# Performance work log

Measured on AMD Instinct MI355X. Metric: run time of the kernel, lower is better.

Reference implementation:

```python
import jax, jax.numpy as jnp
import numpy as np

B, N = 256, 65536          # batch, num_tokens (world.num_tokens == N)
VOCAB = 50257
ALPHA = 0.5                # dirichlet concentration
EPS = 1e-7                 # gumbel eps


def setup_inputs() -> dict:
    key = jax.random.key(0)
    kb, kt, ku, kd = jax.random.split(key, 4)
    batch = jax.random.randint(kb, (B, N), 0, VOCAB, dtype=jnp.int32)
    t = jax.random.uniform(kt, (B,), dtype=jnp.float32)
    U = jax.random.uniform(ku, (B, N), dtype=jnp.float32)
    # dirichlet(alpha=0.5) sample over the token axis, one simplex per row
    D = jax.random.dirichlet(kd, ALPHA * jnp.ones((N,), jnp.float32), shape=(B,)).astype(jnp.float32)
    return {"batch": batch, "t": t, "U": U, "D": D}


def cosine_schedule(t):
    return 1.0 - jnp.cos(jnp.pi * t / 2)


def cosine_weight(t, eps=1e-3):
    t_adj = t * (1 - 2 * eps) + eps
    return 0.5 * jnp.pi * jnp.sin(jnp.pi * t_adj / 2)


def binary_topk(weights, ks):
    # weights: [B, N] float; ks: [B, 1] int -> bool mask marking the top-k per row
    Bn, Nn = weights.shape
    idx = jnp.argsort(-weights, axis=-1)                     # descending order indices
    rank = jnp.broadcast_to(jnp.arange(Nn), (Bn, Nn))        # rank of each sorted slot
    mask = jnp.zeros((Bn, Nn), dtype=bool)
    mask = mask.at[jnp.arange(Bn)[:, None], idx].set(ks > rank)
    return mask


def reference(batch, t, U, D):
    r = cosine_schedule(t)                                   # mask rate per sample [B]
    w = cosine_weight(t)                                     # loss weight per sample [B]
    G = -jnp.log(-jnp.log(U + EPS) + EPS)                    # gumbel noise [B, N]
    weights = G + jnp.log(D)                                 # gumbel + log-dirichlet
    ks = (N * r).astype(jnp.int32)[:, None]                  # [B, 1] tokens to mask
    mask = binary_topk(weights, ks)                          # [B, N] bool
    return mask, w
```

## Files before the change

kernel.cpp:

```cpp
#include <hip/hip_runtime.h>
#include <math.h>

#define BB 256
#define NN 65536
#define NT 1024
#define CAP 2016
#define MARGIN 2e-3f

typedef float f32x4 __attribute__((ext_vector_type(4)));
typedef unsigned int u32x4 __attribute__((ext_vector_type(4)));

#define ONE_BITS 0x3F800000u

__device__ __forceinline__ unsigned int f2sort(float f) {
    unsigned int b = __float_as_uint(f);
    return (b & 0x80000000u) ? ~b : (b | 0x80000000u);
}
__device__ __forceinline__ float sort2f(unsigned int u) {
    unsigned int b = (u & 0x80000000u) ? (u & 0x7fffffffu) : ~u;
    return __uint_as_float(b);
}

__device__ __forceinline__ unsigned int wexact(float u, float d) {
    float t1 = u + 1e-7f;
    float t2 = (float)log((double)t1);
    float t3 = (-t2) + 1e-7f;
    float G  = -(float)log((double)t3);
    float lgD = (float)log((double)d);
    return f2sort(G + lgD);
}

__device__ __forceinline__ unsigned int wfast(float u, float d) {
    float t1 = u + 1e-7f;
    float t3 = -__logf(t1) + 1e-7f;
    float G  = -__logf(t3);
    return f2sort(G + __logf(d));
}

__device__ __forceinline__ bool finite_f(float f) {
    return (__float_as_uint(f) & 0x7f800000u) != 0x7f800000u;
}

#define PASS1SEL(KKV) \
    { const int b0 = tid * 8; unsigned int cs = 0; \
      _Pragma("unroll") for (int i = 0; i < 8; i++) cs += hist[b0 + i]; \
      chunkSum[tid] = cs; } \
    __syncthreads(); \
    if (tid < 64) { \
        const int c0i = lane * 16; unsigned int s = 0; \
        _Pragma("unroll") for (int i = 0; i < 16; i++) s += chunkSum[c0i + i]; \
        unsigned int suf = s; \
        _Pragma("unroll") for (int off = 1; off < 64; off <<= 1) { \
            unsigned int tv = __shfl_down(suf, off); if (lane + off < 64) suf += tv; } \
        unsigned int above = suf - s; \
        if (suf >= (KKV) && above < (KKV)) { \
            unsigned int cum = above; \
            for (int ci = c0i + 15; ci >= c0i; ci--) { \
                unsigned int cch = chunkSum[ci]; \
                if (cum + cch >= (KKV)) { \
                    for (int b = ci * 8 + 7; ; b--) { \
                        unsigned int c2 = hist[b]; \
                        if (cum + c2 >= (KKV)) { s_sel = (unsigned int)b; s_kneed = (KKV) - cum; s_eq = c2; break; } \
                        cum += c2; } \
                    break; } \
                cum += cch; } } } \
    __syncthreads();

#define PASS2SEL(P, KN) \
    if (tid < 64) { \
        const int c0i = lane * 16; unsigned int s = 0; \
        _Pragma("unroll") for (int i = 0; i < 16; i++) s += hist[c0i + i]; \
        unsigned int suf = s; \
        _Pragma("unroll") for (int off = 1; off < 64; off <<= 1) { \
            unsigned int tv = __shfl_down(suf, off); if (lane + off < 64) suf += tv; } \
        unsigned int above = suf - s; \
        if (suf >= (KN) && above < (KN)) { \
            unsigned int cum = above; \
            for (int b = c0i + 15; ; b--) { \
                unsigned int c2 = hist[b]; \
                if (cum + c2 >= (KN)) { s_sel = ((P) << 10) | (unsigned int)b; s_kneed = (KN) - cum; s_eq = c2; break; } \
                cum += c2; } } } \
    __syncthreads();

#define PASS3SEL(P, KN) \
    if (tid < 64) { \
        const int c0i = lane * 8; unsigned int s = 0; \
        _Pragma("unroll") for (int i = 0; i < 8; i++) s += hist[c0i + i]; \
        unsigned int suf = s; \
        _Pragma("unroll") for (int off = 1; off < 64; off <<= 1) { \
            unsigned int tv = __shfl_down(suf, off); if (lane + off < 64) suf += tv; } \
        unsigned int above = suf - s; \
        if (suf >= (KN) && above < (KN)) { \
            unsigned int cum = above; \
            for (int b = c0i + 7; ; b--) { \
                unsigned int c2 = hist[b]; \
                if (cum + c2 >= (KN)) { s_sel = ((P) << 9) | (unsigned int)b; s_kneed = (KN) - cum; s_eq = c2; break; } \
                cum += c2; } } } \
    __syncthreads();

__global__ __launch_bounds__(NT, 4)
void md_fused_kernel(const float* __restrict__ Tt,
                     const float* __restrict__ U,
                     const float* __restrict__ D,
                     float* __restrict__ out,
                     float* __restrict__ wout) {
    const int row = blockIdx.x;
    const int tid = threadIdx.x;
    const int lane = tid & 63;

    const float* Ur = U + (size_t)row * NN;
    const float* Dr = D + (size_t)row * NN;
    unsigned int* OrU = (unsigned int*)out + (size_t)row * NN;

    __shared__ unsigned int hist[8192];
    __shared__ unsigned int chunkSum[NT];
    __shared__ unsigned int bandU[CAP];
    __shared__ int bandIdx[CAP];
    __shared__ unsigned int s_sel, s_kneed, s_eq;
    __shared__ int s_A, s_bandCnt, s_tiecnt, s_tieidx;

    int* tielist = bandIdx;

    const float t = Tt[row];
    const float pf = (float)M_PI;
    float aa = pf * t;
    float bbv = aa * 0.5f;
    float c0 = (float)cos((double)bbv);
    float r  = 1.0f - c0;
    const int k = (int)(65536.0f * r);
    if (tid == 0) {
        float tadj = t * 0.998f + 0.001f;
        float arg  = (pf * tadj) * 0.5f;
        wout[row] = (float)(0.5 * M_PI) * (float)sin((double)arg);
    }

    if (k <= 0 || k >= NN) {
        const unsigned int fb = (k >= NN) ? ONE_BITS : 0u;
        u32x4 f4 = {fb, fb, fb, fb};
        for (int j = 0; j < 16; j++)
            __builtin_nontemporal_store(f4, (u32x4*)(OrU + j * 4096 + tid * 4));
        return;
    }
    const unsigned int kk = (unsigned int)k;

    for (int i = tid; i < 8192; i += NT) hist[i] = 0;
    if (tid == 0) { s_A = 0; s_bandCnt = 0; }
    __syncthreads();

#pragma unroll 2
    for (int J = 0; J < 16; ++J) {
        const int e = (J << 12) + (tid << 2);
        float4 u4 = *(const float4*)(Ur + e);
        float4 d4 = *(const float4*)(Dr + e);
        u32x4 kv;
        kv.x = wfast(u4.x, d4.x);
        kv.y = wfast(u4.y, d4.y);
        kv.z = wfast(u4.z, d4.z);
        kv.w = wfast(u4.w, d4.w);
        *(u32x4*)(OrU + e) = kv;
        atomicAdd(&hist[kv.x >> 19], 1u);
        atomicAdd(&hist[kv.y >> 19], 1u);
        atomicAdd(&hist[kv.z >> 19], 1u);
        atomicAdd(&hist[kv.w >> 19], 1u);
    }
    __syncthreads();

    PASS1SEL(kk)
    const unsigned int p13 = s_sel;
    const unsigned int kn1 = s_kneed;
    hist[tid] = 0;
    __syncthreads();

#pragma unroll 2
    for (int J = 0; J < 16; ++J) {
        const int e = (J << 12) + (tid << 2);
        u32x4 kv = *(const u32x4*)(OrU + e);
        if ((kv.x >> 19) == p13) atomicAdd(&hist[(kv.x >> 9) & 1023u], 1u);
        if ((kv.y >> 19) == p13) atomicAdd(&hist[(kv.y >> 9) & 1023u], 1u);
        if ((kv.z >> 19) == p13) atomicAdd(&hist[(kv.z >> 9) & 1023u], 1u);
        if ((kv.w >> 19) == p13) atomicAdd(&hist[(kv.w >> 9) & 1023u], 1u);
    }
    __syncthreads();
    PASS2SEL(p13, kn1)

    const unsigned int p23 = s_sel;
    const float loF = sort2f(p23 << 9) - MARGIN;
    const float hiF = sort2f((p23 << 9) | 511u) + MARGIN;
    const bool badBand = !(finite_f(loF) && finite_f(hiF));
    const unsigned int lo_u = f2sort(loF);
    const unsigned int hi_u = f2sort(hiF);

    {
        int cnt = 0;
#pragma unroll 2
        for (int J = 0; J < 16; ++J) {
            const int e = (J << 12) + (tid << 2);
            u32x4 kv = __builtin_nontemporal_load((const u32x4*)(OrU + e));
            u32x4 m;
#define MRGV(UU, EIDX, MF) { const unsigned int uu = (UU); \
            const bool din = uu > hi_u; cnt += (int)din; MF = din ? ONE_BITS : 0u; \
            if (!din && uu >= lo_u) { \
                int slot = atomicAdd(&s_bandCnt, 1); \
                if (slot < CAP) bandIdx[slot] = (EIDX); } }
            MRGV(kv.x, e + 0, m.x)
            MRGV(kv.y, e + 1, m.y)
            MRGV(kv.z, e + 2, m.z)
            MRGV(kv.w, e + 3, m.w)
#undef MRGV
            __builtin_nontemporal_store(m, (u32x4*)(OrU + e));
        }
#pragma unroll
        for (int off = 32; off >= 1; off >>= 1) cnt += __shfl_down(cnt, off);
        if (lane == 0) atomicAdd(&s_A, cnt);
    }
    __syncthreads();

    const int bandCnt = s_bandCnt;
    const int kb = k - s_A;
    const bool fallback = badBand || (bandCnt > CAP) || (kb < 0) || (kb > bandCnt);

    if (!fallback) {
        for (int j = tid; j < bandCnt; j += NT) {
            int idx = bandIdx[j];
            bandU[j] = wexact(Ur[idx], Dr[idx]);
        }
        __syncthreads();
        for (int j = tid; j < bandCnt; j += NT) {
            unsigned int me = bandU[j];
            int mi = bandIdx[j];
            int rk = 0;
            for (int i = 0; i < bandCnt; i++) {
                unsigned int o = bandU[i];
                rk += (int)((o > me) || (o == me && bandIdx[i] < mi));
            }
            if (rk < kb) OrU[mi] = ONE_BITS;
        }
        return;
    }

    __syncthreads();
    for (int i = tid; i < 8192; i += NT) hist[i] = 0;
    __syncthreads();
#pragma unroll 1
    for (int J = 0; J < 16; ++J) {
        const int e = (J << 12) + (tid << 2);
        float4 u4 = *(const float4*)(Ur + e);
        float4 d4 = *(const float4*)(Dr + e);
        u32x4 kv;
        kv.x = wexact(u4.x, d4.x);
        kv.y = wexact(u4.y, d4.y);
        kv.z = wexact(u4.z, d4.z);
        kv.w = wexact(u4.w, d4.w);
        *(u32x4*)(OrU + e) = kv;
        atomicAdd(&hist[kv.x >> 19], 1u);
        atomicAdd(&hist[kv.y >> 19], 1u);
        atomicAdd(&hist[kv.z >> 19], 1u);
        atomicAdd(&hist[kv.w >> 19], 1u);
    }
    __syncthreads();

    PASS1SEL(kk)
    const unsigned int q13 = s_sel;
    const unsigned int en1 = s_kneed;
    hist[tid] = 0;
    __syncthreads();
#pragma unroll 1
    for (int J = 0; J < 16; ++J) {
        const int e = (J << 12) + (tid << 2);
        u32x4 kv = *(const u32x4*)(OrU + e);
        if ((kv.x >> 19) == q13) atomicAdd(&hist[(kv.x >> 9) & 1023u], 1u);
        if ((kv.y >> 19) == q13) atomicAdd(&hist[(kv.y >> 9) & 1023u], 1u);
        if ((kv.z >> 19) == q13) atomicAdd(&hist[(kv.z >> 9) & 1023u], 1u);
        if ((kv.w >> 19) == q13) atomicAdd(&hist[(kv.w >> 9) & 1023u], 1u);
    }
    __syncthreads();
    PASS2SEL(q13, en1)

    const unsigned int q23 = s_sel;
    const unsigned int en2 = s_kneed;
    if (tid < 512) hist[tid] = 0;
    __syncthreads();
#pragma unroll 1
    for (int J = 0; J < 16; ++J) {
        const int e = (J << 12) + (tid << 2);
        u32x4 kv = *(const u32x4*)(OrU + e);
        if ((kv.x >> 9) == q23) atomicAdd(&hist[kv.x & 511u], 1u);
        if ((kv.y >> 9) == q23) atomicAdd(&hist[kv.y & 511u], 1u);
        if ((kv.z >> 9) == q23) atomicAdd(&hist[kv.z & 511u], 1u);
        if ((kv.w >> 9) == q23) atomicAdd(&hist[kv.w & 511u], 1u);
    }
    __syncthreads();
    PASS3SEL(q23, en2)

    const unsigned int theta = s_sel;
    const unsigned int kneedF = s_kneed, eqF = s_eq;
    const bool needOrder = (kneedF < eqF);
    int istar = NN;
    if (needOrder) {
        if (tid == 0) s_tiecnt = 0;
        __syncthreads();
#pragma unroll 1
        for (int J = 0; J < 16; ++J) {
            const int e = (J << 12) + (tid << 2);
            u32x4 kv = *(const u32x4*)(OrU + e);
#define TIEV(UU, EIDX) if ((UU) == theta) { \
                int pos = atomicAdd(&s_tiecnt, 1); \
                if (pos < 1024) tielist[pos] = (EIDX); }
            TIEV(kv.x, e + 0)
            TIEV(kv.y, e + 1)
            TIEV(kv.z, e + 2)
            TIEV(kv.w, e + 3)
#undef TIEV
        }
        __syncthreads();
        if (tid == 0) {
            int E = s_tiecnt; if (E > 1024) E = 1024;
            for (int aI = 1; aI < E; aI++) {
                int val = tielist[aI]; int bI = aI - 1;
                while (bI >= 0 && tielist[bI] > val) { tielist[bI + 1] = tielist[bI]; bI--; }
                tielist[bI + 1] = val;
            }
            int kk2 = (int)kneedF; if (kk2 > E) kk2 = E; if (kk2 < 1) kk2 = 1;
            s_tieidx = tielist[kk2 - 1];
        }
        __syncthreads();
        istar = s_tieidx;
    }

#pragma unroll 1
    for (int J = 0; J < 16; ++J) {
        const int e = (J << 12) + (tid << 2);
        u32x4 kv = __builtin_nontemporal_load((const u32x4*)(OrU + e));
        u32x4 m;
#define MVE(u, idx) ((((u) > theta) || ((u) == theta && (!needOrder || (idx) <= istar))) ? ONE_BITS : 0u)
        m.x = MVE(kv.x, e + 0);
        m.y = MVE(kv.y, e + 1);
        m.z = MVE(kv.z, e + 2);
        m.w = MVE(kv.w, e + 3);
#undef MVE
        __builtin_nontemporal_store(m, (u32x4*)(OrU + e));
    }
}

extern "C" void kernel_launch(void* const* d_in, const int* in_sizes, int n_in,
                              void* d_out, int out_size, void* d_ws, size_t ws_size,
                              hipStream_t stream) {
    const float* T = (const float*)d_in[1];
    const float* U = (const float*)d_in[2];
    const float* D = (const float*)d_in[3];
    float* out = (float*)d_out;
    float* wout = out + (size_t)BB * NN;

    md_fused_kernel<<<BB, NT, 0, stream>>>(T, U, D, out, wout);
}
```

Baseline: 233.5 us.

## Select top-k via sampled pivots and monotone ratio key with candidate compaction

Replaces the gumbel+log-dirichlet key with a monotone-equivalent ratio key d/(-log(u)) that needs only one fast log and a reciprocal. Instead of two full passes writing and rereading keys in global memory, it samples the first 4096 elements to estimate high and low rank pivots, then makes one streaming pass that writes the mask for definitely-selected elements and wave-compacts candidates into shared memory. Exact selection within the candidates uses a radix select followed by an exact-key brute-force rank on a narrow band. This removes global key writes and rereads but adds sampling overhead and more fallback conditions. It also relies on the sample being representative.

```diff
diff --git a/kernel.cpp b/kernel.cpp
--- a/kernel.cpp
+++ b/kernel.cpp
@@ -4,8 +4,11 @@
 #define BB 256
 #define NN 65536
 #define NT 1024
-#define CAP 2016
-#define MARGIN 2e-3f
+#define SM 4096
+#define RANKPAD 160
+#define CAPC 8192
+#define CAPB 2048
+#define QMARG 2e-3f
 
 typedef float f32x4 __attribute__((ext_vector_type(4)));
 typedef unsigned int u32x4 __attribute__((ext_vector_type(4)));
@@ -30,11 +33,10 @@
     return f2sort(G + lgD);
 }
 
-__device__ __forceinline__ unsigned int wfast(float u, float d) {
-    float t1 = u + 1e-7f;
-    float t3 = -__logf(t1) + 1e-7f;
-    float G  = -__logf(t3);
-    return f2sort(G + __logf(d));
+__device__ __forceinline__ unsigned int qkey(float u, float d) {
+    float t3 = 1e-7f - __logf(u + 1e-7f);
+    float q  = d * __builtin_amdgcn_rcpf(t3);
+    return f2sort(q);
 }
 
 __device__ __forceinline__ bool finite_f(float f) {
@@ -114,12 +116,15 @@
 
     __shared__ unsigned int hist[8192];
     __shared__ unsigned int chunkSum[NT];
-    __shared__ unsigned int bandU[CAP];
-    __shared__ int bandIdx[CAP];
+    __shared__ unsigned int skey[SM];
+    __shared__ unsigned int candKey[CAPC];
+    __shared__ int candIdx[CAPC];
     __shared__ unsigned int s_sel, s_kneed, s_eq;
-    __shared__ int s_A, s_bandCnt, s_tiecnt, s_tieidx;
-
-    int* tielist = bandIdx;
+    __shared__ int s_A, s_candCnt, s_bandCnt, s_above, s_tiecnt, s_tieidx;
+
+    unsigned int* bandU = skey;
+    int* bandIdxA = (int*)(skey + CAPB);
+    int* tielist = candIdx;
 
     const float t = Tt[row];
     const float pf = (float)M_PI;
@@ -135,8 +140,8 @@
     }
 
     if (k <= 0 || k >= NN) {
-        const unsigned int fb = (k >= NN) ? ONE_BITS : 0u;
-        u32x4 f4 = {fb, fb, fb, fb};
+        const unsigned int fbv = (k >= NN) ? ONE_BITS : 0u;
+        u32x4 f4 = {fbv, fbv, fbv, fbv};
         for (int j = 0; j < 16; j++)
             __builtin_nontemporal_store(f4, (u32x4*)(OrU + j * 4096 + tid * 4));
         return;
@@ -144,98 +149,168 @@
     const unsigned int kk = (unsigned int)k;
 
     for (int i = tid; i < 8192; i += NT) hist[i] = 0;
-    if (tid == 0) { s_A = 0; s_bandCnt = 0; }
-    __syncthreads();
-
-#pragma unroll 2
-    for (int J = 0; J < 16; ++J) {
-        const int e = (J << 12) + (tid << 2);
-        float4 u4 = *(const float4*)(Ur + e);
-        float4 d4 = *(const float4*)(Dr + e);
-        u32x4 kv;
-        kv.x = wfast(u4.x, d4.x);
-        kv.y = wfast(u4.y, d4.y);
-        kv.z = wfast(u4.z, d4.z);
-        kv.w = wfast(u4.w, d4.w);
-        *(u32x4*)(OrU + e) = kv;
-        atomicAdd(&hist[kv.x >> 19], 1u);
-        atomicAdd(&hist[kv.y >> 19], 1u);
-        atomicAdd(&hist[kv.z >> 19], 1u);
-        atomicAdd(&hist[kv.w >> 19], 1u);
-    }
-    __syncthreads();
-
-    PASS1SEL(kk)
-    const unsigned int p13 = s_sel;
-    const unsigned int kn1 = s_kneed;
-    hist[tid] = 0;
-    __syncthreads();
-
-#pragma unroll 2
-    for (int J = 0; J < 16; ++J) {
-        const int e = (J << 12) + (tid << 2);
-        u32x4 kv = *(const u32x4*)(OrU + e);
-        if ((kv.x >> 19) == p13) atomicAdd(&hist[(kv.x >> 9) & 1023u], 1u);
-        if ((kv.y >> 19) == p13) atomicAdd(&hist[(kv.y >> 9) & 1023u], 1u);
-        if ((kv.z >> 19) == p13) atomicAdd(&hist[(kv.z >> 9) & 1023u], 1u);
-        if ((kv.w >> 19) == p13) atomicAdd(&hist[(kv.w >> 9) & 1023u], 1u);
-    }
-    __syncthreads();
-    PASS2SEL(p13, kn1)
-
-    const unsigned int p23 = s_sel;
-    const float loF = sort2f(p23 << 9) - MARGIN;
-    const float hiF = sort2f((p23 << 9) | 511u) + MARGIN;
-    const bool badBand = !(finite_f(loF) && finite_f(hiF));
-    const unsigned int lo_u = f2sort(loF);
-    const unsigned int hi_u = f2sort(hiF);
-
+    if (tid == 0) { s_A = 0; s_candCnt = 0; s_bandCnt = 0; s_above = 0; }
+    __syncthreads();
     {
-        int cnt = 0;
+        float4 u4 = *(const float4*)(Ur + (tid << 2));
+        float4 d4 = *(const float4*)(Dr + (tid << 2));
+        unsigned int s0 = qkey(u4.x, d4.x), s1 = qkey(u4.y, d4.y);
+        unsigned int s2 = qkey(u4.z, d4.z), s3 = qkey(u4.w, d4.w);
+        skey[(tid << 2) + 0] = s0; skey[(tid << 2) + 1] = s1;
+        skey[(tid << 2) + 2] = s2; skey[(tid << 2) + 3] = s3;
+        atomicAdd(&hist[s0 >> 19], 1u); atomicAdd(&hist[s1 >> 19], 1u);
+        atomicAdd(&hist[s2 >> 19], 1u); atomicAdd(&hist[s3 >> 19], 1u);
+    }
+    __syncthreads();
+
+    const int rh = (k >> 4) - RANKPAD;
+    unsigned int hi_pivot_u = 0xFFFFFFFFu;
+    if (rh >= 1) {
+        PASS1SEL((unsigned int)rh)
+        const unsigned int bh = s_sel; const unsigned int knh = s_kneed;
+        hist[tid] = 0;
+        __syncthreads();
+        for (int j = tid; j < SM; j += NT) { unsigned int sk = skey[j];
+            if ((sk >> 19) == bh) atomicAdd(&hist[(sk >> 9) & 1023u], 1u); }
+        __syncthreads();
+        PASS2SEL(bh, knh)
+        hi_pivot_u = (s_sel << 9) | 0x1FFu;
+        for (int i = tid; i < 8192; i += NT) hist[i] = 0;
+        __syncthreads();
+        for (int j = tid; j < SM; j += NT) atomicAdd(&hist[skey[j] >> 19], 1u);
+        __syncthreads();
+    }
+
+    const int rl = ((k + 15) >> 4) + RANKPAD;
+    unsigned int lo_pivot_u = 0u;
+    if (rl <= SM) {
+        PASS1SEL((unsigned int)rl)
+        const unsigned int bl = s_sel; const unsigned int knl = s_kneed;
+        hist[tid] = 0;
+        __syncthreads();
+        for (int j = tid; j < SM; j += NT) { unsigned int sk = skey[j];
+            if ((sk >> 19) == bl) atomicAdd(&hist[(sk >> 9) & 1023u], 1u); }
+        __syncthreads();
+        PASS2SEL(bl, knl)
+        lo_pivot_u = (s_sel << 9);
+    }
+    __syncthreads();
+
+    {
+        int cntA = 0;
 #pragma unroll 2
         for (int J = 0; J < 16; ++J) {
             const int e = (J << 12) + (tid << 2);
-            u32x4 kv = __builtin_nontemporal_load((const u32x4*)(OrU + e));
+            float4 u4 = *(const float4*)(Ur + e);
+            float4 d4 = *(const float4*)(Dr + e);
+            u32x4 kv;
+            kv.x = qkey(u4.x, d4.x); kv.y = qkey(u4.y, d4.y);
+            kv.z = qkey(u4.z, d4.z); kv.w = qkey(u4.w, d4.w);
             u32x4 m;
-#define MRGV(UU, EIDX, MF) { const unsigned int uu = (UU); \
-            const bool din = uu > hi_u; cnt += (int)din; MF = din ? ONE_BITS : 0u; \
-            if (!din && uu >= lo_u) { \
-                int slot = atomicAdd(&s_bandCnt, 1); \
-                if (slot < CAP) bandIdx[slot] = (EIDX); } }
-            MRGV(kv.x, e + 0, m.x)
-            MRGV(kv.y, e + 1, m.y)
-            MRGV(kv.z, e + 2, m.z)
-            MRGV(kv.w, e + 3, m.w)
-#undef MRGV
-            __builtin_nontemporal_store(m, (u32x4*)(OrU + e));
+#define MPROC(KC, CI, MF) { \
+            const unsigned int qv = (KC); \
+            const bool din = qv > hi_pivot_u; \
+            cntA += (int)din; MF = din ? ONE_BITS : 0u; \
+            const bool isc = (!din) && (qv > lo_pivot_u); \
+            const unsigned long long mb = __ballot(isc); \
+            if (mb) { \
+                const int ldr = __ffsll((unsigned long long)mb) - 1; \
+                int wbase = 0; \
+                if (lane == ldr) wbase = atomicAdd(&s_candCnt, __popcll(mb)); \
+                wbase = __shfl(wbase, ldr); \
+                if (isc) { \
+                    const int slot = wbase + __popcll(mb & ((1ull << lane) - 1ull)); \
+                    if (slot < CAPC) { candKey[slot] = qv; candIdx[slot] = e + (CI); } \
+                } } }
+            MPROC(kv.x, 0, m.x)
+            MPROC(kv.y, 1, m.y)
+            MPROC(kv.z, 2, m.z)
+            MPROC(kv.w, 3, m.w)
+#undef MPROC
+            *(u32x4*)(OrU + e) = m;
         }
 #pragma unroll
-        for (int off = 32; off >= 1; off >>= 1) cnt += __shfl_down(cnt, off);
-        if (lane == 0) atomicAdd(&s_A, cnt);
-    }
-    __syncthreads();
-
-    const int bandCnt = s_bandCnt;
+        for (int off = 32; off >= 1; off >>= 1) cntA += __shfl_down(cntA, off);
+        if (lane == 0) atomicAdd(&s_A, cntA);
+    }
+    __syncthreads();
+
+    const int candCnt0 = s_candCnt;
+    const int candCnt = candCnt0 > CAPC ? CAPC : candCnt0;
     const int kb = k - s_A;
-    const bool fallback = badBand || (bandCnt > CAP) || (kb < 0) || (kb > bandCnt);
-
-    if (!fallback) {
-        for (int j = tid; j < bandCnt; j += NT) {
-            int idx = bandIdx[j];
-            bandU[j] = wexact(Ur[idx], Dr[idx]);
+    bool fb = (candCnt0 > CAPC) || (kb < 1) || (kb > candCnt0);
+
+    unsigned int theta_q = 0, band_lo_u = 0, band_hi_u = 0;
+    if (!fb) {
+        for (int i = tid; i < 8192; i += NT) hist[i] = 0;
+        __syncthreads();
+        for (int j = tid; j < candCnt; j += NT) atomicAdd(&hist[candKey[j] >> 19], 1u);
+        __syncthreads();
+        PASS1SEL((unsigned int)kb)
+        const unsigned int c13 = s_sel; const unsigned int ck1 = s_kneed;
+        hist[tid] = 0;
+        __syncthreads();
+        for (int j = tid; j < candCnt; j += NT) { unsigned int ck = candKey[j];
+            if ((ck >> 19) == c13) atomicAdd(&hist[(ck >> 9) & 1023u], 1u); }
+        __syncthreads();
+        PASS2SEL(c13, ck1)
+        const unsigned int c23 = s_sel; const unsigned int ck2 = s_kneed;
+        if (tid < 512) hist[tid] = 0;
+        __syncthreads();
+        for (int j = tid; j < candCnt; j += NT) { unsigned int ck = candKey[j];
+            if ((ck >> 9) == c23) atomicAdd(&hist[ck & 511u], 1u); }
+        __syncthreads();
+        PASS3SEL(c23, ck2)
+        theta_q = s_sel;
+
+        const float theta_f = sort2f(theta_q);
+        band_lo_u = f2sort(theta_f * (1.0f - QMARG));
+        band_hi_u = f2sort(theta_f * (1.0f + QMARG));
+        { const unsigned int fl = (theta_q >= 0x80000100u) ? (theta_q - 256u) : 0x80000000u;
+          if (band_lo_u > fl) band_lo_u = fl;
+          const unsigned int fh = theta_q + 256u;
+          if (band_hi_u < fh) band_hi_u = fh; }
+        fb = !(finite_f(theta_f)) || !(band_hi_u < hi_pivot_u) || !(band_lo_u > lo_pivot_u);
+    }
+
+    if (!fb) {
+        int ab = 0;
+        for (int j = tid; j < candCnt; j += NT) {
+            const unsigned int ck = candKey[j];
+            if (ck > band_hi_u) ab++;
+            else if (ck >= band_lo_u) {
+                const int slot = atomicAdd(&s_bandCnt, 1);
+                if (slot < CAPB) bandIdxA[slot] = candIdx[j];
+            }
         }
-        __syncthreads();
-        for (int j = tid; j < bandCnt; j += NT) {
-            unsigned int me = bandU[j];
-            int mi = bandIdx[j];
-            int rk = 0;
-            for (int i = 0; i < bandCnt; i++) {
-                unsigned int o = bandU[i];
-                rk += (int)((o > me) || (o == me && bandIdx[i] < mi));
+#pragma unroll
+        for (int off = 32; off >= 1; off >>= 1) ab += __shfl_down(ab, off);
+        if (lane == 0) atomicAdd(&s_above, ab);
+        __syncthreads();
+        const int bandCnt = s_bandCnt;
+        const int kb2 = kb - s_above;
+        fb = (bandCnt > CAPB) || (kb2 < 0) || (kb2 > bandCnt);
+
+        if (!fb) {
+            for (int j = tid; j < bandCnt; j += NT) {
+                const int idx = bandIdxA[j];
+                bandU[j] = wexact(Ur[idx], Dr[idx]);
             }
-            if (rk < kb) OrU[mi] = ONE_BITS;
+            __syncthreads();
+            for (int j = tid; j < bandCnt; j += NT) {
+                const unsigned int me = bandU[j];
+                const int mi = bandIdxA[j];
+                int rk = 0;
+                for (int i = 0; i < bandCnt; i++) {
+                    const unsigned int o = bandU[i];
+                    rk += (int)((o > me) || (o == me && bandIdxA[i] < mi));
+                }
+                if (rk < kb2) OrU[mi] = ONE_BITS;
+            }
+            for (int j = tid; j < candCnt; j += NT)
+                if (candKey[j] > band_hi_u) OrU[candIdx[j]] = ONE_BITS;
+            return;
         }
-        return;
     }
 
     __syncthreads();
@@ -330,7 +405,7 @@
 #pragma unroll 1
     for (int J = 0; J < 16; ++J) {
         const int e = (J << 12) + (tid << 2);
-        u32x4 kv = __builtin_nontemporal_load((const u32x4*)(OrU + e));
+        u32x4 kv = *(const u32x4*)(OrU + e);
         u32x4 m;
 #define MVE(u, idx) ((((u) > theta) || ((u) == theta && (!needOrder || (idx) <= istar))) ? ONE_BITS : 0u)
         m.x = MVE(kv.x, e + 0);
@@ -338,7 +413,7 @@
         m.z = MVE(kv.z, e + 2);
         m.w = MVE(kv.w, e + 3);
 #undef MVE
-        __builtin_nontemporal_store(m, (u32x4*)(OrU + e));
+        *(u32x4*)(OrU + e) = m;
     }
 }
 
```

Result: no change. 230.4 us (-1.3%).
